# Kernel tuning notes

Measured on AMD Instinct MI355X. Metric: run time of the kernel, lower is better.

## Reference

```python
import jax, jax.numpy as jnp
import numpy as np

B, M, F = 32, 32768, 256


def setup_inputs() -> dict:
    key = jax.random.key(0)
    ks = jax.random.split(key, 6)
    scale1 = 1.0 / np.sqrt(2 * F)
    scale2 = 1.0 / np.sqrt(F)
    return {
        "input_data": jax.random.normal(ks[0], (B, F), dtype=jnp.float32),
        "memory": jax.random.normal(ks[1], (M, F), dtype=jnp.float32),
        "W1": jax.random.uniform(ks[2], (F, 2 * F), jnp.float32, -scale1, scale1),
        "b1": jax.random.uniform(ks[3], (F,), jnp.float32, -scale1, scale1),
        "W2": jax.random.uniform(ks[4], (1, F), jnp.float32, -scale2, scale2),
        "b2": jax.random.uniform(ks[5], (1,), jnp.float32, -scale2, scale2),
        # threshold below 1/M so the conditional scatter-write path actually fires
        # (torch default 0.05 with random weights never writes for M=32768)
        "threshold": jnp.float32(1e-5),
    }


def reference(input_data, memory, W1, b1, W2, b2, threshold):
    # Linear on cat([x, mem]) splits into two independent matmuls.
    W1x, W1m = W1[:, :F], W1[:, F:]          # each [F, F]
    hx = input_data @ W1x.T                   # [B, F]
    hm = memory @ W1m.T                       # [M, F]
    h = jnp.tanh(hx[:, None, :] + hm[None, :, :] + b1)  # [B, M, F]
    scores = h @ W2[0] + b2[0]                # [B, M]
    weights = jax.nn.softmax(scores, axis=1)  # softmax over memory slots
    best = jnp.argmax(weights, axis=1)        # [B] winning slot per item
    maxw = jnp.max(weights, axis=1)           # [B]
    mask = maxw > threshold                   # write only if above threshold
    # Sequential loop semantics: later batch items overwrite earlier ones
    # at the same slot. last[s] = 1 + index of last masked writer to slot s.
    order = jnp.where(mask, jnp.arange(B, dtype=jnp.int32) + 1, 0)
    last = jax.ops.segment_max(order, best, num_segments=M)  # [M]
    last = jnp.maximum(last, 0)
    src = input_data[jnp.maximum(last - 1, 0)]               # [M, F]
    updated_memory = jnp.where((last > 0)[:, None], src, memory)
    return updated_memory
```

## Files before the change

kernel.cpp:

```cpp
#include <hip/hip_runtime.h>

#define FDIM 256
#define BDIM 32
#define MDIM 32768
#define NB   512

#define WS_EM    0
#define WS_EX    (WS_EM + MDIM*FDIM)
#define WS_W2N   (WS_EX + BDIM*FDIM)
#define WS_PMAX  (WS_W2N + FDIM)
#define WS_PSUM  (WS_PMAX + BDIM*NB)
#define WS_PARG  (WS_PSUM + BDIM*NB)
#define WS_WIN   (WS_PARG + BDIM*NB)
#define WS_BEST  (WS_WIN + 32)
#define WS_GMAX  (WS_BEST + 32)
#define WS_GSUM  (WS_GMAX + 32)
#define WS_GARG  (WS_GSUM + 32)
#define WS_WH    (WS_GARG + 32)
#define WS_WL    (WS_WH + 32768)

#define C2 2.8853900817779268f

typedef __attribute__((ext_vector_type(8))) short bf16x8;
typedef __attribute__((ext_vector_type(8))) unsigned short ushort8;
typedef __attribute__((ext_vector_type(4))) float f32x4;

__device__ inline unsigned short f2bf(float x) {
  unsigned u = __float_as_uint(x);
  return (unsigned short)((u + 0x7fffu + ((u >> 16) & 1u)) >> 16);
}
__device__ inline float bf2f(unsigned short h) {
  return __uint_as_float(((unsigned)h) << 16);
}

__global__ __launch_bounds__(256) void k1_prep(const float* __restrict__ input,
                                               const float* __restrict__ W1,
                                               const float* __restrict__ b1,
                                               const float* __restrict__ W2,
                                               float* __restrict__ Ex,
                                               float* __restrict__ w2n,
                                               unsigned short* __restrict__ wh,
                                               unsigned short* __restrict__ wl) {
  if (blockIdx.x < BDIM) {
    const int b = blockIdx.x, f = threadIdx.x;
    const float* in = input + b * FDIM;
    const float* w  = W1 + (size_t)f * 512;
    float acc = b1[f];
    #pragma unroll 8
    for (int k = 0; k < FDIM; k += 4) {
      float4 iv = *(const float4*)(in + k);
      float4 wv = *(const float4*)(w + k);
      acc = fmaf(iv.x, wv.x, acc); acc = fmaf(iv.y, wv.y, acc);
      acc = fmaf(iv.z, wv.z, acc); acc = fmaf(iv.w, wv.w, acc);
    }
    Ex[b * FDIM + f] = __builtin_amdgcn_exp2f(acc * C2);
    if (b == 0) w2n[f] = -2.0f * W2[f];
  } else {
    int id = ((blockIdx.x - BDIM) * 256 + threadIdx.x) * 4;
    int f = id >> 8, c = id & 255;
    float4 v = *(const float4*)(W1 + (size_t)f * 512 + 256 + c);
    float xs[4] = {v.x, v.y, v.z, v.w};
    #pragma unroll
    for (int e = 0; e < 4; ++e) {
      unsigned short h = f2bf(xs[e]);
      wh[id + e] = h;
      wl[id + e] = f2bf(xs[e] - bf2f(h));
    }
  }
}

__global__ __launch_bounds__(512, 4) void k23_fused(const float* __restrict__ mem,
                                                    const unsigned short* __restrict__ wh,
                                                    const unsigned short* __restrict__ wl,
                                                    const float* __restrict__ Ex,
                                                    const float* __restrict__ w2n,
                                                    float* __restrict__ pmax,
                                                    float* __restrict__ psum,
                                                    int* __restrict__ parg,
                                                    float* __restrict__ out) {
  __shared__ __align__(16) char smem[69632];
  unsigned short* AH = (unsigned short*)(smem);
  unsigned short* AL = (unsigned short*)(smem + 5120);
  unsigned short* BH = (unsigned short*)(smem + 10240);
  unsigned short* BL = (unsigned short*)(smem + 30720);
  float* emT = (float*)smem;

  const int tid = threadIdx.x;
  const int lane = tid & 63, wid = tid >> 6;
  const int m0 = blockIdx.x * 64;
  const int rb = lane & 15, g8 = (lane >> 4) * 8;
  const int mh = wid & 1;
  const int fq = wid >> 1;

  f32x4 acc[2][4];
  #pragma unroll
  for (int i = 0; i < 2; ++i)
    #pragma unroll
    for (int j = 0; j < 4; ++j) acc[i][j] = (f32x4){0.f, 0.f, 0.f, 0.f};

  for (int s = 0; s < 8; ++s) {
    const int k0 = s * 32;
    __syncthreads();
    if (tid < 256) {
      int r = tid >> 2, c8 = (tid & 3) * 8;
      float4 a0 = *(const float4*)(mem + (size_t)(m0 + r) * 256 + k0 + c8);
      float4 a1 = *(const float4*)(mem + (size_t)(m0 + r) * 256 + k0 + c8 + 4);
      float xs[8] = {a0.x, a0.y, a0.z, a0.w, a1.x, a1.y, a1.z, a1.w};
      ushort8 ahv, alv;
      #pragma unroll
      for (int e = 0; e < 8; ++e) {
        unsigned short h = f2bf(xs[e]);
        ahv[e] = h;
        alv[e] = f2bf(xs[e] - bf2f(h));
      }
      *(ushort8*)&AH[r * 40 + c8] = ahv;
      *(ushort8*)&AL[r * 40 + c8] = alv;
    } else {
      int t2 = tid - 256;
      #pragma unroll
      for (int q = 0; q < 4; ++q) {
        int id = q * 256 + t2, br = id >> 2, bc = (id & 3) * 8;
        *(uint4*)&BH[br * 40 + bc] = *(const uint4*)(wh + (size_t)br * 256 + k0 + bc);
        *(uint4*)&BL[br * 40 + bc] = *(const uint4*)(wl + (size_t)br * 256 + k0 + bc);
      }
    }
    __syncthreads();

    bf16x8 fah[2], fal[2], fbh[4], fbl[4];
    #pragma unroll
    for (int i = 0; i < 2; ++i) {
      fah[i] = *(const bf16x8*)&AH[(mh * 32 + i * 16 + rb) * 40 + g8];
      fal[i] = *(const bf16x8*)&AL[(mh * 32 + i * 16 + rb) * 40 + g8];
    }
    #pragma unroll
    for (int j = 0; j < 4; ++j) {
      fbh[j] = *(const bf16x8*)&BH[(fq * 64 + j * 16 + rb) * 40 + g8];
      fbl[j] = *(const bf16x8*)&BL[(fq * 64 + j * 16 + rb) * 40 + g8];
    }
    #pragma unroll
    for (int i = 0; i < 2; ++i)
      #pragma unroll
      for (int j = 0; j < 4; ++j) {
        acc[i][j] = __builtin_amdgcn_mfma_f32_16x16x32_bf16(fah[i], fbh[j], acc[i][j], 0, 0, 0);
        acc[i][j] = __builtin_amdgcn_mfma_f32_16x16x32_bf16(fah[i], fbl[j], acc[i][j], 0, 0, 0);
        acc[i][j] = __builtin_amdgcn_mfma_f32_16x16x32_bf16(fal[i], fbh[j], acc[i][j], 0, 0, 0);
      }
  }

  __syncthreads();
  #pragma unroll
  for (int j = 0; j < 4; ++j)
    #pragma unroll
    for (int i = 0; i < 2; ++i) {
      const int fl = fq * 64 + j * 16 + rb;
      const int mloc = mh * 32 + i * 16 + (lane >> 4) * 4;
      float4 v;
      v.x = __builtin_amdgcn_exp2f(acc[i][j][0] * C2);
      v.y = __builtin_amdgcn_exp2f(acc[i][j][1] * C2);
      v.z = __builtin_amdgcn_exp2f(acc[i][j][2] * C2);
      v.w = __builtin_amdgcn_exp2f(acc[i][j][3] * C2);
      *(float4*)(emT + fl * 68 + mloc) = v;
    }
  __syncthreads();

  const int wuid = __builtin_amdgcn_readfirstlane(wid);
  const float* ex0 = Ex + (size_t)(wuid * 4 + 0) * FDIM;
  const float* ex1 = Ex + (size_t)(wuid * 4 + 1) * FDIM;
  const float* ex2 = Ex + (size_t)(wuid * 4 + 2) * FDIM;
  const float* ex3 = Ex + (size_t)(wuid * 4 + 3) * FDIM;

  float acc0 = 0.f, acc1 = 0.f, acc2 = 0.f, acc3 = 0.f;
  #pragma unroll 8
  for (int f = 0; f < FDIM; ++f) {
    float em = emT[f * 68 + lane];
    float w  = w2n[f];
    float u;
    u = fmaf(em, ex0[f], 1.f); acc0 = fmaf(w, __builtin_amdgcn_rcpf(u), acc0);
    u = fmaf(em, ex1[f], 1.f); acc1 = fmaf(w, __builtin_amdgcn_rcpf(u), acc1);
    u = fmaf(em, ex2[f], 1.f); acc2 = fmaf(w, __builtin_amdgcn_rcpf(u), acc2);
    u = fmaf(em, ex3[f], 1.f); acc3 = fmaf(w, __builtin_amdgcn_rcpf(u), acc3);
  }

  float accb[4] = {acc0, acc1, acc2, acc3};
  const int blk = blockIdx.x;
  #pragma unroll
  for (int bi = 0; bi < 4; ++bi) {
    float s = accb[bi]; int idx = m0 + lane;
    #pragma unroll
    for (int off = 32; off > 0; off >>= 1) {
      float so = __shfl_xor(s, off);
      int   io = __shfl_xor(idx, off);
      if (so > s || (so == s && io < idx)) { s = so; idx = io; }
    }
    float ex = __expf(accb[bi] - s);
    #pragma unroll
    for (int off = 32; off > 0; off >>= 1) ex += __shfl_xor(ex, off);
    if (lane == 0) {
      int b = wuid * 4 + bi;
      pmax[b * NB + blk] = s;
      psum[b * NB + blk] = ex;
      parg[b * NB + blk] = idx;
    }
  }

  {
    const float4* src = (const float4*)(mem + (size_t)m0 * FDIM);
    float4* dst = (float4*)(out + (size_t)m0 * FDIM);
    #pragma unroll
    for (int i = 0; i < 8; ++i) dst[tid + i * 512] = src[tid + i * 512];
  }
}

__global__ __launch_bounds__(256) void k4a_reduce(const float* __restrict__ pmax,
                                                  const float* __restrict__ psum,
                                                  const int* __restrict__ parg,
                                                  float* __restrict__ gmax,
                                                  float* __restrict__ gsum,
                                                  int* __restrict__ garg) {
  __shared__ float sm[4], ss[4];
  __shared__ int   sa[4];
  const int b = blockIdx.x, tid = threadIdx.x;
  float cm = -3.0e38f, cs = 0.f; int ca = 0x7fffffff;
  #pragma unroll
  for (int t = 0; t < NB / 256; ++t) {
    int i = t * 256 + tid;
    float s = pmax[b * NB + i];
    float p = psum[b * NB + i];
    int   a = parg[b * NB + i];
    if (s > cm)      { cs = cs * __expf(cm - s) + p; cm = s; ca = a; }
    else if (s == cm){ cs += p; if (a < ca) ca = a; }
    else             { cs += p * __expf(s - cm); }
  }
  #pragma unroll
  for (int off = 32; off > 0; off >>= 1) {
    float om = __shfl_xor(cm, off);
    float os = __shfl_xor(cs, off);
    int   oa = __shfl_xor(ca, off);
    if (om > cm)      { cs = cs * __expf(cm - om) + os; cm = om; ca = oa; }
    else if (om == cm){ cs += os; if (oa < ca) ca = oa; }
    else              { cs += os * __expf(om - cm); }
  }
  if ((tid & 63) == 0) { sm[tid >> 6] = cm; ss[tid >> 6] = cs; sa[tid >> 6] = ca; }
  __syncthreads();
  if (tid == 0) {
    cm = sm[0]; cs = ss[0]; ca = sa[0];
    for (int w = 1; w < 4; ++w) {
      float om = sm[w], os = ss[w]; int oa = sa[w];
      if (om > cm)      { cs = cs * __expf(cm - om) + os; cm = om; ca = oa; }
      else if (om == cm){ cs += os; if (oa < ca) ca = oa; }
      else              { cs += os * __expf(om - cm); }
    }
    gmax[b] = cm; gsum[b] = cs; garg[b] = ca;
  }
}

__global__ __launch_bounds__(64) void k4b_select(const float* __restrict__ gsum,
                                                 const int* __restrict__ garg,
                                                 const float* __restrict__ thr_p,
                                                 int* __restrict__ win,
                                                 int* __restrict__ best) {
  const int tid = threadIdx.x;
  if (tid < BDIM) {
    const float thr = *thr_p;
    int me = garg[tid];
    int w = (1.0f / gsum[tid] > thr) ? 1 : 0;
    if (w) {
      for (int b2 = tid + 1; b2 < BDIM; ++b2)
        if ((1.0f / gsum[b2] > thr) && garg[b2] == me) { w = 0; break; }
    }
    win[tid] = w; best[tid] = me;
  }
}

__global__ __launch_bounds__(64) void k6_patch(const float* __restrict__ input,
                                               const int* __restrict__ win,
                                               const int* __restrict__ best,
                                               float* __restrict__ out) {
  const int b = blockIdx.x;
  if (!win[b]) return;
  const int m = best[b];
  const int t = threadIdx.x;
  *(float4*)(out + (size_t)m * 256 + t * 4) = *(const float4*)(input + (size_t)b * 256 + t * 4);
}

extern "C" void kernel_launch(void* const* d_in, const int* in_sizes, int n_in,
                              void* d_out, int out_size, void* d_ws, size_t ws_size,
                              hipStream_t stream) {
  const float* input  = (const float*)d_in[0];
  const float* memory = (const float*)d_in[1];
  const float* W1     = (const float*)d_in[2];
  const float* b1     = (const float*)d_in[3];
  const float* W2     = (const float*)d_in[4];
  const float* thr    = (const float*)d_in[6];

  float* ws   = (float*)d_ws;
  float* Ex   = ws + WS_EX;
  float* w2n  = ws + WS_W2N;
  float* pmax = ws + WS_PMAX;
  float* psum = ws + WS_PSUM;
  int*   parg = (int*)(ws + WS_PARG);
  int*   win  = (int*)(ws + WS_WIN);
  int*   best = (int*)(ws + WS_BEST);
  float* gmax = ws + WS_GMAX;
  float* gsum = ws + WS_GSUM;
  int*   garg = (int*)(ws + WS_GARG);
  unsigned short* wh = (unsigned short*)(ws + WS_WH);
  unsigned short* wl = (unsigned short*)(ws + WS_WL);
  float* out  = (float*)d_out;

  hipLaunchKernelGGL(k1_prep,    dim3(BDIM + 64), dim3(256), 0, stream, input, W1, b1, W2, Ex, w2n, wh, wl);
  hipLaunchKernelGGL(k23_fused,  dim3(MDIM / 64), dim3(512), 0, stream, memory, wh, wl, Ex, w2n, pmax, psum, parg, out);
  hipLaunchKernelGGL(k4a_reduce, dim3(BDIM),      dim3(256), 0, stream, pmax, psum, parg, gmax, gsum, garg);
  hipLaunchKernelGGL(k4b_select, dim3(1),         dim3(64),  0, stream, gsum, garg, thr, win, best);
  hipLaunchKernelGGL(k6_patch,   dim3(BDIM),      dim3(64),  0, stream, input, win, best, out);
}
```

Measured before the change: 76.60 us.

## Combine four reciprocals into one and fuse memory copy into tile loads

The score loop now sums four w/u terms using a common denominator, so it issues one reciprocal per four features instead of four. This removes transcendental (rcp) throughput pressure at the cost of extra multiplies, and the product of four denominators could overflow or lose precision. Separately, the copy of memory to the output is moved into the staging loads that already read each memory tile. That drops the second global read of the block's rows at the end of the kernel.

New measurement: 71.71 us. -6.4%, faster.

```diff
diff --git a/kernel.cpp b/kernel.cpp
--- a/kernel.cpp
+++ b/kernel.cpp
@@ -103,8 +103,12 @@
     __syncthreads();
     if (tid < 256) {
       int r = tid >> 2, c8 = (tid & 3) * 8;
-      float4 a0 = *(const float4*)(mem + (size_t)(m0 + r) * 256 + k0 + c8);
-      float4 a1 = *(const float4*)(mem + (size_t)(m0 + r) * 256 + k0 + c8 + 4);
+      const float* mrow = mem + (size_t)(m0 + r) * 256 + k0 + c8;
+      float4 a0 = *(const float4*)(mrow);
+      float4 a1 = *(const float4*)(mrow + 4);
+      float* orow = out + (size_t)(m0 + r) * 256 + k0 + c8;
+      *(float4*)(orow)     = a0;
+      *(float4*)(orow + 4) = a1;
       float xs[8] = {a0.x, a0.y, a0.z, a0.w, a1.x, a1.y, a1.z, a1.w};
       ushort8 ahv, alv;
       #pragma unroll
@@ -170,15 +174,32 @@
   const float* ex3 = Ex + (size_t)(wuid * 4 + 3) * FDIM;
 
   float acc0 = 0.f, acc1 = 0.f, acc2 = 0.f, acc3 = 0.f;
-  #pragma unroll 8
-  for (int f = 0; f < FDIM; ++f) {
-    float em = emT[f * 68 + lane];
-    float w  = w2n[f];
-    float u;
-    u = fmaf(em, ex0[f], 1.f); acc0 = fmaf(w, __builtin_amdgcn_rcpf(u), acc0);
-    u = fmaf(em, ex1[f], 1.f); acc1 = fmaf(w, __builtin_amdgcn_rcpf(u), acc1);
-    u = fmaf(em, ex2[f], 1.f); acc2 = fmaf(w, __builtin_amdgcn_rcpf(u), acc2);
-    u = fmaf(em, ex3[f], 1.f); acc3 = fmaf(w, __builtin_amdgcn_rcpf(u), acc3);
+  #pragma unroll 2
+  for (int f = 0; f < FDIM; f += 4) {
+    float e0 = emT[(f + 0) * 68 + lane];
+    float e1 = emT[(f + 1) * 68 + lane];
+    float e2 = emT[(f + 2) * 68 + lane];
+    float e3 = emT[(f + 3) * 68 + lane];
+    float w0 = w2n[f + 0], w1 = w2n[f + 1];
+    float w2 = w2n[f + 2], w3 = w2n[f + 3];
+    #define SCORE4(exP, accV)                                            \
+    {                                                                    \
+      float u0 = fmaf(e0, exP[f + 0], 1.f);                              \
+      float u1 = fmaf(e1, exP[f + 1], 1.f);                              \
+      float u2 = fmaf(e2, exP[f + 2], 1.f);                              \
+      float u3 = fmaf(e3, exP[f + 3], 1.f);                              \
+      float p01 = u0 * u1, p23 = u2 * u3;                                \
+      float den = p01 * p23;                                             \
+      float t0 = fmaf(w1, u0, w0 * u1);                                  \
+      float t1 = fmaf(w3, u2, w2 * u3);                                  \
+      float num = fmaf(t1, p01, t0 * p23);                               \
+      accV = fmaf(num, __builtin_amdgcn_rcpf(den), accV);                \
+    }
+    SCORE4(ex0, acc0)
+    SCORE4(ex1, acc1)
+    SCORE4(ex2, acc2)
+    SCORE4(ex3, acc3)
+    #undef SCORE4
   }
 
   float accb[4] = {acc0, acc1, acc2, acc3};
@@ -201,13 +222,6 @@
       psum[b * NB + blk] = ex;
       parg[b * NB + blk] = idx;
     }
-  }
-
-  {
-    const float4* src = (const float4*)(mem + (size_t)m0 * FDIM);
-    float4* dst = (float4*)(out + (size_t)m0 * FDIM);
-    #pragma unroll
-    for (int i = 0; i < 8; ++i) dst[tid + i * 512] = src[tid + i * 512];
   }
 }
 
```
